# Optimization experiments

Hardware: AMD Instinct MI355X
Metric: run time of the kernel (lower is better)

The kernel has to match this reference:

```python
import jax, jax.numpy as jnp
import numpy as np

BOUND = 1.0
N_RAYS = 2048
TOT = 128        # num_steps (samples per pixel)
IND_S = 16       # indicator_steps
MAX_DEPTHS = 2
HID = 64
EPS = 1e-8


def setup_inputs() -> dict:
    key = jax.random.key(0)
    ks = jax.random.split(key, 13)
    M = N_RAYS * TOT
    rays_o = 0.3 * jax.random.normal(ks[0], (N_RAYS, 3), jnp.float32)
    rd = jax.random.normal(ks[1], (N_RAYS, 3), jnp.float32)
    rays_d = rd / (jnp.linalg.norm(rd, axis=-1, keepdims=True) + EPS)
    env_map = 0.1 * jax.random.normal(ks[2], (3, 128, 256), jnp.float32)
    Wd1 = jax.random.normal(ks[3], (3, HID), jnp.float32) / np.sqrt(3.0)
    Wd2 = jax.random.normal(ks[4], (HID, 3), jnp.float32) / np.sqrt(HID)
    Wf1 = jax.random.normal(ks[5], (6, HID), jnp.float32) / np.sqrt(6.0)
    Ws = jax.random.normal(ks[6], (HID, 3), jnp.float32) / np.sqrt(HID)
    Wdir = jax.random.normal(ks[7], (HID, 3), jnp.float32) / np.sqrt(HID)
    Wrho = jax.random.normal(ks[8], (HID, 3), jnp.float32) / np.sqrt(HID)
    jitter = jax.random.uniform(ks[9], (MAX_DEPTHS, M, IND_S), jnp.float32)
    u_t = jax.random.uniform(ks[10], (MAX_DEPTHS, M), jnp.float32)
    u_scatter = jax.random.uniform(ks[11], (MAX_DEPTHS, M), jnp.float32)
    channel = jax.random.randint(ks[12], (MAX_DEPTHS, M), 0, 3)
    return dict(rays_o=rays_o, rays_d=rays_d, env_map=env_map, Wd1=Wd1, Wd2=Wd2,
                Wf1=Wf1, Ws=Ws, Wdir=Wdir, Wrho=Wrho,
                jitter=jitter, u_t=u_t, u_scatter=u_scatter, channel=channel)


def _density(pts, Wd1, Wd2):
    # stand-in NeRF density field: 3 spectral channels, positive
    return jax.nn.softplus(jnp.sin(pts @ Wd1) @ Wd2)


def _material(o, d, Wf1, Ws, Wdir, Wrho):
    f = jnp.tanh(jnp.concatenate([o, d], axis=-1) @ Wf1)
    sigma_t = jax.nn.softplus(f @ Ws)                     # [M,3]
    dn = f @ Wdir
    d_out = dn / (jnp.linalg.norm(dn, axis=-1, keepdims=True) + EPS)
    fused_rho = jax.nn.sigmoid(f @ Wrho)                  # [M,3]
    return sigma_t, d_out, fused_rho


def _sample_env(env_map, p):
    # equirectangular lookup == torch grid_sample(bilinear, align_corners=False, zero pad)
    x, y, z = p[:, 0], p[:, 1], p[:, 2]
    theta = jnp.nan_to_num(jnp.arctan2(x, -z)) / jnp.pi            # grid x in [-1,1]
    phi = 2.0 / jnp.pi * jnp.nan_to_num(jnp.arccos(y)) - 1.0       # grid y in [-1,1]
    C, H, W = env_map.shape
    ix = ((theta + 1.0) * W - 1.0) * 0.5
    iy = ((phi + 1.0) * H - 1.0) * 0.5
    x0 = jnp.floor(ix); y0 = jnp.floor(iy)
    wx = ix - x0; wy = iy - y0

    def tap(xc, yc, w):
        inb = (xc >= 0) & (xc < W) & (yc >= 0) & (yc < H)
        xi = jnp.clip(xc, 0, W - 1).astype(jnp.int32)
        yi = jnp.clip(yc, 0, H - 1).astype(jnp.int32)
        return (w * inb)[:, None] * env_map[:, yi, xi].T   # [M,3]

    v = (tap(x0, y0, (1 - wx) * (1 - wy)) + tap(x0 + 1, y0, wx * (1 - wy)) +
         tap(x0, y0 + 1, (1 - wx) * wy) + tap(x0 + 1, y0 + 1, wx * wy))
    return jnp.exp(v)


def _render(rays_o, rays_d, env_map, Wd1, Wd2, Wf1, Ws, Wdir, Wrho,
            jitter, u_t, u_scatter, channel):
    M = N_RAYS * TOT
    o = jnp.repeat(rays_o, TOT, axis=0)   # [M,3]
    d = jnp.repeat(rays_d, TOT, axis=0)
    alive = jnp.ones((M,), bool)          # masked version of boolean compaction
    thr = jnp.ones((M, 3), jnp.float32)
    rgbs = jnp.zeros((M, 3), jnp.float32)
    lin = jnp.linspace(0.0, 1.0, IND_S)

    for dep in range(MAX_DEPTHS):
        # ray-sphere intersection (radius=bound)
        a = jnp.sum(d * d, -1)
        b = 2.0 * jnp.sum(d * o, -1)
        c = jnp.sum(o * o, -1) - BOUND ** 2
        delta = b * b - 4.0 * a * c
        alive = alive & (delta > 0.0)
        sq = jnp.sqrt(jnp.maximum(delta, 0.0))
        nears = jnp.maximum((-b - sq) / (2.0 * a), 0.001)
        fars = jnp.maximum((-b + sq) / (2.0 * a), 0.001)
        span = fars - nears

        # stratified indicator samples -> per-channel majorant
        z = nears[:, None] + span[:, None] * lin[None, :]
        z = z + (jitter[dep] - 0.5) * (span[:, None] / IND_S)
        pts = o[:, None, :] + d[:, None, :] * z[:, :, None]          # [M,S,3]
        sigma = _density(pts.reshape(-1, 3), Wd1, Wd2).reshape(M, IND_S, 3)
        ch = channel[dep]
        maj_multi = jnp.maximum(sigma.max(axis=1), 0.001)            # [M,3]
        sig_ch = jnp.take_along_axis(sigma, ch[:, None, None], axis=2)[..., 0]
        maj = jnp.maximum(sig_ch.max(axis=1), 0.001)                 # [M]

        # free-flight sampling (last depth forces hit at far boundary)
        if dep < MAX_DEPTHS - 1:
            t = -jnp.log1p(-u_t[dep]) / maj + nears
        else:
            t = fars
        hit = alive & (t >= fars)

        # environment hit contribution
        denom = jnp.exp(-maj_multi * span[:, None]) / (maj_multi.max(-1, keepdims=True) + EPS) + EPS
        Le = _sample_env(env_map, o + d * fars[:, None])
        contrib = thr * (denom / jax.lax.stop_gradient(denom.mean(-1, keepdims=True))) * Le
        rgbs = rgbs + jnp.where(hit[:, None], contrib, 0.0)
        alive = alive & ~hit
        if dep == MAX_DEPTHS - 1:
            break

        # throughput update + null/real scattering (delta tracking)
        trans = jnp.exp(-maj_multi * (t - nears)[:, None]) / maj_multi.max(-1, keepdims=True)
        den2 = jax.lax.stop_gradient((maj_multi * trans).mean(-1, keepdims=True))
        thr = jnp.where(alive[:, None], thr * trans / den2, thr)
        o = jnp.where(alive[:, None], jax.lax.stop_gradient(o + d * t[:, None]), o)
        sigma_t, d_out, fused_rho = _material(o, d, Wf1, Ws, Wdir, Wrho)
        sp = jnp.minimum(jnp.take_along_axis(sigma_t, ch[:, None], axis=1)[:, 0] / maj, 1.0)
        sm = alive & (u_scatter[dep] < sp)
        d = jnp.where(sm[:, None], d_out, d)
        thr = jnp.where(sm[:, None], thr / (sp[:, None] + EPS) * fused_rho,
              jnp.where(alive[:, None], thr / (1.0 - sp[:, None] + EPS), thr))

    return rgbs.reshape(N_RAYS, TOT, 3).mean(axis=1)   # [N,3]


def reference(rays_o, rays_d, env_map, Wd1, Wd2, Wf1, Ws, Wdir, Wrho,
              jitter, u_t, u_scatter, channel):
    return _render(rays_o, rays_d, env_map, Wd1, Wd2, Wf1, Ws, Wdir, Wrho,
                   jitter, u_t, u_scatter, channel)
```

## Files before the change

### kernel.cpp

```cpp
#include <hip/hip_runtime.h>
#include <math.h>

#define NRAYS 2048
#define TOT   128
#define INDS  16
#define HID   64
#define EPSF  1e-8f
#define MTOT  (NRAYS*TOT)
#define NTAB  128

typedef float f32x2 __attribute__((ext_vector_type(2)));
typedef float f32x4 __attribute__((ext_vector_type(4)));

__device__ __forceinline__ float rcp_f(float x) {
    return __builtin_amdgcn_rcpf(x);
}
__device__ __forceinline__ float softplus_f(float x) {
    return fmaxf(x, 0.0f) + __logf(1.0f + __expf(-fabsf(x)));
}
__device__ __forceinline__ float sigmoid_f(float x) {
    return rcp_f(1.0f + __expf(-x));
}
__device__ __forceinline__ float tanh_fast(float x) {
    float e2 = __expf(2.0f * x);
    return 1.0f - 2.0f * rcp_f(e2 + 1.0f);
}
__device__ __forceinline__ f32x2 pkmax(f32x2 a, f32x2 b) {
    f32x2 r; r.x = fmaxf(a.x, b.x); r.y = fmaxf(a.y, b.y); return r;
}
__device__ __forceinline__ f32x2 pkfma(f32x2 a, f32x2 b, f32x2 c) {
    return __builtin_elementwise_fma(a, b, c);
}

__device__ __forceinline__ float atan_poly(float r) {
    float r2 = r*r;
    float p = -0.0117212f;
    p = fmaf(p, r2,  0.05265332f);
    p = fmaf(p, r2, -0.11643287f);
    p = fmaf(p, r2,  0.19354346f);
    p = fmaf(p, r2, -0.33262347f);
    p = fmaf(p, r2,  0.99997726f);
    return r * p;
}
__device__ __forceinline__ float atan2_fast(float y, float x) {
    float ay = fabsf(y), ax = fabsf(x);
    float mx = fmaxf(ay, ax), mn = fminf(ay, ax);
    float r  = mn * rcp_f(fmaxf(mx, 1e-30f));
    float t  = atan_poly(r);
    t = (ay > ax) ? (1.57079632679f - t) : t;
    t = (x < 0.0f) ? (3.14159265359f - t) : t;
    return (y < 0.0f) ? -t : t;
}
__device__ __forceinline__ float acos_fast(float x) {
    float ax = fabsf(x);
    float p = -0.0187293f;
    p = fmaf(p, ax,  0.0742610f);
    p = fmaf(p, ax, -0.2121144f);
    p = fmaf(p, ax,  1.5707288f);
    float s = sqrtf(1.0f - ax) * p;
    return (x < 0.0f) ? (3.14159265359f - s) : s;
}

#define CK(i) ((float)(i)*(1.0f/15.0f) - 0.03125f)

#define MAKE_Z(jA, jB, kbase, nears, span)                                    \
    float s16 = (span) * (1.0f/16.0f);                                        \
    f32x2 z01, z23, z45, z67;                                                 \
    z01.x = fmaf((jA).x, s16, fmaf(span, CK((kbase)+0), nears));              \
    z01.y = fmaf((jA).y, s16, fmaf(span, CK((kbase)+1), nears));              \
    z23.x = fmaf((jA).z, s16, fmaf(span, CK((kbase)+2), nears));              \
    z23.y = fmaf((jA).w, s16, fmaf(span, CK((kbase)+3), nears));              \
    z45.x = fmaf((jB).x, s16, fmaf(span, CK((kbase)+4), nears));              \
    z45.y = fmaf((jB).y, s16, fmaf(span, CK((kbase)+5), nears));              \
    z67.x = fmaf((jB).z, s16, fmaf(span, CK((kbase)+6), nears));              \
    z67.y = fmaf((jB).w, s16, fmaf(span, CK((kbase)+7), nears));

#define TAB_EVAL(zz, mx0, mx1, mx2)                                           \
    {                                                                         \
        float x = ((zz) - ztab0) * invh;                                      \
        x = fminf(fmaxf(x, 0.0f), (float)(NTAB-1) - 1e-3f);                   \
        int i = (int)x; float w = x - (float)i;                               \
        float ta0 = sT0[i], tb0 = sT0[i+1];                                   \
        float ta1 = sT1[i], tb1 = sT1[i+1];                                   \
        float ta2 = sT2[i], tb2 = sT2[i+1];                                   \
        mx0 = fmaxf(mx0, fmaf(w, tb0 - ta0, ta0));                            \
        mx1 = fmaxf(mx1, fmaf(w, tb1 - ta1, ta1));                            \
        mx2 = fmaxf(mx2, fmaf(w, tb2 - ta2, ta2));                            \
    }

__device__ __forceinline__ void env_logv(
    const float* __restrict__ env_map,
    float px, float py, float pz,
    float& v0, float& v1, float& v2)
{
    float theta = atan2_fast(px, -pz) * (1.0f/3.14159265358979323846f);
    float acv = (fabsf(py) <= 1.0f) ? acos_fast(py) : 0.0f;
    float phi = 0.63661977236758134308f * acv - 1.0f;
    float ixf = ((theta + 1.0f)*256.0f - 1.0f)*0.5f;
    float iyf = ((phi   + 1.0f)*128.0f - 1.0f)*0.5f;
    float x0f = floorf(ixf), y0f = floorf(iyf);
    float wx = ixf - x0f, wy = iyf - y0f;
    v0 = 0.f; v1 = 0.f; v2 = 0.f;
    auto tap = [&](float xc, float yc, float w) {
        if (xc >= 0.0f && xc < 256.0f && yc >= 0.0f && yc < 128.0f) {
            int xi = (int)xc, yi = (int)yc;
            const float* e = env_map + yi*256 + xi;
            v0 += w * e[0];
            v1 += w * e[128*256];
            v2 += w * e[2*128*256];
        }
    };
    tap(x0f,      y0f,      (1.0f-wx)*(1.0f-wy));
    tap(x0f+1.0f, y0f,      wx*(1.0f-wy));
    tap(x0f,      y0f+1.0f, (1.0f-wx)*wy);
    tap(x0f+1.0f, y0f+1.0f, wx*wy);
}

__global__ __launch_bounds__(256)
void render_kernel(const float* __restrict__ rays_o,
                   const float* __restrict__ rays_d,
                   const float* __restrict__ env_map,
                   const float* __restrict__ Wd1,
                   const float* __restrict__ Wd2,
                   const float* __restrict__ Wf1,
                   const float* __restrict__ Ws,
                   const float* __restrict__ Wdir,
                   const float* __restrict__ Wrho,
                   const float* __restrict__ jitter,
                   const float* __restrict__ u_t,
                   const float* __restrict__ u_scatter,
                   const int*   __restrict__ channel,
                   float* __restrict__ out)
{
    const int ray  = blockIdx.x;
    const int tid  = threadIdx.x;
    const int s    = tid >> 1;
    const int half = tid & 1;
    const int m    = ray * TOT + s;
    const int kbase = half * 8;

    __shared__ f32x4 sAB[HID];
    __shared__ f32x4 sW01[HID];
    __shared__ f32x2 sW2[HID];
    __shared__ f32x4 sPW[HID];
    __shared__ f32x4 sM0[HID];
    __shared__ f32x4 sM1[HID];
    __shared__ f32x4 sM2[HID];
    __shared__ float sT0[NTAB];
    __shared__ float sT1[NTAB];
    __shared__ float sT2[NTAB];
    __shared__ f32x4 sP0[TOT];
    __shared__ f32x4 sP1[TOT];
    __shared__ f32x2 sP2[TOT];
    __shared__ float sEnvE[3];
    __shared__ int   sCnt;
    __shared__ float sred[4][3];

    const float4* j0p = (const float4*)(jitter + (size_t)m*INDS + kbase);
    float4 j0A = j0p[0], j0B = j0p[1];
    const float4* j1p = (const float4*)(jitter + ((size_t)MTOT + m)*INDS + kbase);
    float4 j1A = j1p[0], j1B = j1p[1];
    int   ch = channel[m];
    float ut = u_t[m];
    float us = u_scatter[m];

    float ox = rays_o[ray*3+0], oy = rays_o[ray*3+1], oz = rays_o[ray*3+2];
    float dx = rays_d[ray*3+0], dy = rays_d[ray*3+1], dz = rays_d[ray*3+2];

    if (tid == 0) sCnt = 0;
    if (tid < HID) {
        const float INV2PI = 0.15915494309189535f;
        float w1x = Wd1[tid], w1y = Wd1[HID+tid], w1z = Wd1[2*HID+tid];
        float pw1x = w1x*INV2PI, pw1y = w1y*INV2PI, pw1z = w1z*INV2PI;
        float A = ox*pw1x + oy*pw1y + oz*pw1z;
        float B = dx*pw1x + dy*pw1y + dz*pw1z;
        float w20 = Wd2[3*tid], w21 = Wd2[3*tid+1], w22 = Wd2[3*tid+2];
        sAB[tid]  = (f32x4){A, A, B, B};
        sW01[tid] = (f32x4){w20, w20, w21, w21};
        sW2[tid]  = (f32x2){w22, w22};
        sPW[tid]  = (f32x4){pw1x, pw1y, pw1z, 0.0f};
        float f0 = Wf1[tid],       f1 = Wf1[HID+tid],   f2 = Wf1[2*HID+tid];
        float f3 = Wf1[3*HID+tid], f4 = Wf1[4*HID+tid], f5 = Wf1[5*HID+tid];
        float P = ox*f0 + oy*f1 + oz*f2 + dx*f3 + dy*f4 + dz*f5;
        float Q = dx*f0 + dy*f1 + dz*f2;
        sM0[tid] = (f32x4){P, Q, Ws[3*tid], Ws[3*tid+1]};
        sM1[tid] = (f32x4){Ws[3*tid+2], Wdir[3*tid], Wdir[3*tid+1], Wdir[3*tid+2]};
        sM2[tid] = (f32x4){Wrho[3*tid], Wrho[3*tid+1], Wrho[3*tid+2], 0.0f};
    }
    __syncthreads();

    float a0g = dx*dx + dy*dy + dz*dz;
    float b0g = 2.0f*(dx*ox + dy*oy + dz*oz);
    float c0g = (ox*ox + oy*oy + oz*oz) - 1.0f;
    float delta0 = b0g*b0g - 4.0f*a0g*c0g;
    bool alive = (delta0 > 0.0f);

    float nears = 0.f, fars = 0.f, span = 0.f, ztab0 = 0.f, invh = 0.f;
    if (alive) {
        float sq = sqrtf(delta0);
        float inv2a = rcp_f(a0g + a0g);
        nears = fmaxf((-b0g - sq) * inv2a, 0.001f);
        fars  = fmaxf((-b0g + sq) * inv2a, 0.001f);
        span  = fars - nears;
        ztab0 = fmaf(-span, 0.03125f, nears);
        float width = span * 1.0625f;
        float hstep = width * (1.0f/(NTAB-1));
        invh = (float)(NTAB-1) * rcp_f(width);
        int p = tid >> 1;
        float zp = fmaf((float)p, hstep, ztab0);
        float f0 = 0.f, f1 = 0.f, f2 = 0.f;
        const int jb = half * 32;
        #pragma unroll 4
        for (int j = jb; j < jb + 32; ++j) {
            f32x4 ab  = sAB[j];
            f32x4 w01 = sW01[j];
            f32x2 w2  = sW2[j];
            float hv = __builtin_amdgcn_sinf(fmaf(zp, ab.z, ab.x));
            f0 = fmaf(hv, w01.x, f0);
            f1 = fmaf(hv, w01.z, f1);
            f2 = fmaf(hv, w2.x, f2);
        }
        f0 += __shfl_xor(f0, 1, 64);
        f1 += __shfl_xor(f1, 1, 64);
        f2 += __shfl_xor(f2, 1, 64);
        if (half == 0) { sT0[p] = f0; sT1[p] = f1; sT2[p] = f2; }
        if (tid == 0) {
            float v0,v1,v2;
            env_logv(env_map, fmaf(dx,fars,ox), fmaf(dy,fars,oy), fmaf(dz,fars,oz),
                     v0,v1,v2);
            sEnvE[0] = __expf(v0); sEnvE[1] = __expf(v1); sEnvE[2] = __expf(v2);
        }
    }
    __syncthreads();

    float thr0 = 1.f, thr1 = 1.f, thr2 = 1.f;
    float rgb0 = 0.f, rgb1 = 0.f, rgb2 = 0.f;
    bool  tab_d1 = false;
    float tadv = 0.f;

    if (alive) {
        MAKE_Z(j0A, j0B, kbase, nears, span)
        float mx0 = -1e30f, mx1 = -1e30f, mx2 = -1e30f;
        TAB_EVAL(z01.x, mx0,mx1,mx2) TAB_EVAL(z01.y, mx0,mx1,mx2)
        TAB_EVAL(z23.x, mx0,mx1,mx2) TAB_EVAL(z23.y, mx0,mx1,mx2)
        TAB_EVAL(z45.x, mx0,mx1,mx2) TAB_EVAL(z45.y, mx0,mx1,mx2)
        TAB_EVAL(z67.x, mx0,mx1,mx2) TAB_EVAL(z67.y, mx0,mx1,mx2)
        mx0 = fmaxf(mx0, __shfl_xor(mx0, 1, 64));
        mx1 = fmaxf(mx1, __shfl_xor(mx1, 1, 64));
        mx2 = fmaxf(mx2, __shfl_xor(mx2, 1, 64));

        float maj0 = fmaxf(softplus_f(mx0), 0.001f);
        float maj1 = fmaxf(softplus_f(mx1), 0.001f);
        float maj2 = fmaxf(softplus_f(mx2), 0.001f);
        float mmax = fmaxf(fmaxf(maj0, maj1), maj2);

        float maj = (ch == 0) ? maj0 : ((ch == 1) ? maj1 : maj2);
        float t   = fmaf(-__logf(1.0f - ut), rcp_f(maj), nears);

        if (t >= fars) {
            float im   = rcp_f(mmax + EPSF);
            float den0 = fmaf(__expf(-maj0*span), im, EPSF);
            float den1 = fmaf(__expf(-maj1*span), im, EPSF);
            float den2 = fmaf(__expf(-maj2*span), im, EPSF);
            float idm = 3.0f * rcp_f(den0+den1+den2);
            rgb0 = den0*idm*sEnvE[0];
            rgb1 = den1*idm*sEnvE[1];
            rgb2 = den2*idm*sEnvE[2];
        } else {
            float tn  = t - nears;
            float imm = rcp_f(mmax);
            float tr0 = __expf(-maj0*tn) * imm;
            float tr1 = __expf(-maj1*tn) * imm;
            float tr2 = __expf(-maj2*tn) * imm;
            float i2m = 3.0f * rcp_f(maj0*tr0 + maj1*tr1 + maj2*tr2);
            thr0 = tr0 * i2m;
            thr1 = tr1 * i2m;
            thr2 = tr2 * i2m;
            ox = fmaf(dx, t, ox); oy = fmaf(dy, t, oy); oz = fmaf(dz, t, oz);

            float st0=0.f, st1=0.f, st2=0.f;
            float dn0=0.f, dn1=0.f, dn2v=0.f;
            float rh0=0.f, rh1=0.f, rh2=0.f;
            const int j0 = half * 32;
            #pragma unroll 2
            for (int j = j0; j < j0 + 32; ++j) {
                f32x4 q0 = sM0[j];
                f32x4 q1 = sM1[j];
                f32x4 q2 = sM2[j];
                float pre = fmaf(t, q0.y, q0.x);
                float f = tanh_fast(pre);
                st0  = fmaf(f, q0.z, st0);
                st1  = fmaf(f, q0.w, st1);
                st2  = fmaf(f, q1.x, st2);
                dn0  = fmaf(f, q1.y, dn0);
                dn1  = fmaf(f, q1.z, dn1);
                dn2v = fmaf(f, q1.w, dn2v);
                rh0  = fmaf(f, q2.x, rh0);
                rh1  = fmaf(f, q2.y, rh1);
                rh2  = fmaf(f, q2.z, rh2);
            }
            st0  += __shfl_xor(st0, 1, 64);
            st1  += __shfl_xor(st1, 1, 64);
            st2  += __shfl_xor(st2, 1, 64);
            dn0  += __shfl_xor(dn0, 1, 64);
            dn1  += __shfl_xor(dn1, 1, 64);
            dn2v += __shfl_xor(dn2v, 1, 64);
            rh0  += __shfl_xor(rh0, 1, 64);
            rh1  += __shfl_xor(rh1, 1, 64);
            rh2  += __shfl_xor(rh2, 1, 64);

            float stch = (ch == 0) ? st0 : ((ch == 1) ? st1 : st2);
            float sp = fminf(softplus_f(stch) * rcp_f(maj), 1.0f);
            if (us < sp) {
                float inr = rcp_f(sqrtf(dn0*dn0 + dn1*dn1 + dn2v*dn2v) + EPSF);
                float ndx = dn0*inr, ndy = dn1*inr, ndz = dn2v*inr;
                float isp = rcp_f(sp + EPSF);
                float t0 = thr0 * isp * sigmoid_f(rh0);
                float t1 = thr1 * isp * sigmoid_f(rh1);
                float t2 = thr2 * isp * sigmoid_f(rh2);
                if (half == 0) {
                    int sl = atomicAdd(&sCnt, 1);
                    sP0[sl] = (f32x4){ox, oy, oz, ndx};
                    sP1[sl] = (f32x4){ndy, ndz, t0, t1};
                    sP2[sl] = (f32x2){t2, (float)m};
                }
            } else {
                float iv = rcp_f(1.0f - sp + EPSF);
                thr0 *= iv; thr1 *= iv; thr2 *= iv;
                tab_d1 = true;
                tadv = t;
            }
        }
    }
    __syncthreads();
    int npool = sCnt;

    if (tab_d1) {
        float fars1 = fmaxf(fars - tadv, 0.001f);
        float span1 = fars1 - 0.001f;
        float n1    = tadv + 0.001f;
        MAKE_Z(j1A, j1B, kbase, n1, span1)
        float mx0 = -1e30f, mx1 = -1e30f, mx2 = -1e30f;
        TAB_EVAL(z01.x, mx0,mx1,mx2) TAB_EVAL(z01.y, mx0,mx1,mx2)
        TAB_EVAL(z23.x, mx0,mx1,mx2) TAB_EVAL(z23.y, mx0,mx1,mx2)
        TAB_EVAL(z45.x, mx0,mx1,mx2) TAB_EVAL(z45.y, mx0,mx1,mx2)
        TAB_EVAL(z67.x, mx0,mx1,mx2) TAB_EVAL(z67.y, mx0,mx1,mx2)
        mx0 = fmaxf(mx0, __shfl_xor(mx0, 1, 64));
        mx1 = fmaxf(mx1, __shfl_xor(mx1, 1, 64));
        mx2 = fmaxf(mx2, __shfl_xor(mx2, 1, 64));

        float maj0 = fmaxf(softplus_f(mx0), 0.001f);
        float maj1 = fmaxf(softplus_f(mx1), 0.001f);
        float maj2 = fmaxf(softplus_f(mx2), 0.001f);
        float mmax = fmaxf(fmaxf(maj0, maj1), maj2);

        float im   = rcp_f(mmax + EPSF);
        float den0 = fmaf(__expf(-maj0*span1), im, EPSF);
        float den1 = fmaf(__expf(-maj1*span1), im, EPSF);
        float den2 = fmaf(__expf(-maj2*span1), im, EPSF);
        float idm = 3.0f * rcp_f(den0+den1+den2);
        rgb0 += thr0 * den0*idm*sEnvE[0];
        rgb1 += thr1 * den1*idm*sEnvE[1];
        rgb2 += thr2 * den2*idm*sEnvE[2];
    }

    {
        const int qlane = tid & 3;
        const int kq    = qlane * 4;
        const float kqf = (float)kq;
        for (int q = tid >> 2; q < npool; q += 64) {
            f32x4 p0 = sP0[q];
            f32x4 p1 = sP1[q];
            f32x2 p2 = sP2[q];
            float pox = p0.x, poy = p0.y, poz = p0.z;
            float pdx = p0.w, pdy = p1.x, pdz = p1.y;
            float pt0 = p1.z, pt1 = p1.w, pt2 = p2.x;
            int   mm  = (int)p2.y;

            const float4* jp = (const float4*)(jitter + ((size_t)MTOT + mm)*INDS + kq);
            float4 jq = jp[0];

            float a1 = pdx*pdx + pdy*pdy + pdz*pdz;
            float b1 = 2.0f*(pdx*pox + pdy*poy + pdz*poz);
            float c1 = (pox*pox + poy*poy + poz*poz) - 1.0f;
            float delta1 = b1*b1 - 4.0f*a1*c1;
            if (delta1 > 0.0f) {
                float sq1    = sqrtf(delta1);
                float inv2a1 = rcp_f(a1 + a1);
                float nears1 = fmaxf((-b1 - sq1) * inv2a1, 0.001f);
                float fars1  = fmaxf((-b1 + sq1) * inv2a1, 0.001f);
                float span1  = fars1 - nears1;
                float s16q   = span1 * (1.0f/16.0f);
                f32x2 zA, zB;
                zA.x = fmaf(jq.x, s16q, fmaf(span1, (kqf+0.0f)*(1.0f/15.0f) - 0.03125f, nears1));
                zA.y = fmaf(jq.y, s16q, fmaf(span1, (kqf+1.0f)*(1.0f/15.0f) - 0.03125f, nears1));
                zB.x = fmaf(jq.z, s16q, fmaf(span1, (kqf+2.0f)*(1.0f/15.0f) - 0.03125f, nears1));
                zB.y = fmaf(jq.w, s16q, fmaf(span1, (kqf+3.0f)*(1.0f/15.0f) - 0.03125f, nears1));

                f32x2 a0A = {0.f,0.f}, a0B = {0.f,0.f};
                f32x2 a1A = {0.f,0.f}, a1B = {0.f,0.f};
                f32x2 a2A = {0.f,0.f}, a2B = {0.f,0.f};
                #pragma unroll 4
                for (int j = 0; j < HID; ++j) {
                    f32x4 pw  = sPW[j];
                    f32x4 w01 = sW01[j];
                    f32x2 w2  = sW2[j];
                    float A = fmaf(pox, pw.x, fmaf(poy, pw.y, poz*pw.z));
                    float B = fmaf(pdx, pw.x, fmaf(pdy, pw.y, pdz*pw.z));
                    f32x2 A2 = {A, A}, B2 = {B, B};
                    f32x2 gA = pkfma(zA, B2, A2);
                    f32x2 gB = pkfma(zB, B2, A2);
                    f32x2 hA, hB;
                    hA.x = __builtin_amdgcn_sinf(gA.x); hA.y = __builtin_amdgcn_sinf(gA.y);
                    hB.x = __builtin_amdgcn_sinf(gB.x); hB.y = __builtin_amdgcn_sinf(gB.y);
                    f32x2 W0 = {w01.x, w01.y}, W1 = {w01.z, w01.w};
                    a0A = pkfma(hA, W0, a0A); a0B = pkfma(hB, W0, a0B);
                    a1A = pkfma(hA, W1, a1A); a1B = pkfma(hB, W1, a1B);
                    a2A = pkfma(hA, w2, a2A); a2B = pkfma(hB, w2, a2B);
                }
                f32x2 pm0 = pkmax(a0A, a0B);
                f32x2 pm1 = pkmax(a1A, a1B);
                f32x2 pm2 = pkmax(a2A, a2B);
                float mx0 = fmaxf(pm0.x, pm0.y);
                float mx1 = fmaxf(pm1.x, pm1.y);
                float mx2 = fmaxf(pm2.x, pm2.y);
                mx0 = fmaxf(mx0, __shfl_xor(mx0, 1, 64));
                mx1 = fmaxf(mx1, __shfl_xor(mx1, 1, 64));
                mx2 = fmaxf(mx2, __shfl_xor(mx2, 1, 64));
                mx0 = fmaxf(mx0, __shfl_xor(mx0, 2, 64));
                mx1 = fmaxf(mx1, __shfl_xor(mx1, 2, 64));
                mx2 = fmaxf(mx2, __shfl_xor(mx2, 2, 64));

                float maj0 = fmaxf(softplus_f(mx0), 0.001f);
                float maj1 = fmaxf(softplus_f(mx1), 0.001f);
                float maj2 = fmaxf(softplus_f(mx2), 0.001f);
                float mmax = fmaxf(fmaxf(maj0, maj1), maj2);

                float im   = rcp_f(mmax + EPSF);
                float den0 = fmaf(__expf(-maj0*span1), im, EPSF);
                float den1 = fmaf(__expf(-maj1*span1), im, EPSF);
                float den2 = fmaf(__expf(-maj2*span1), im, EPSF);
                float idm = 3.0f * rcp_f(den0+den1+den2);
                float v0,v1,v2;
                env_logv(env_map, fmaf(pdx,fars1,pox), fmaf(pdy,fars1,poy),
                         fmaf(pdz,fars1,poz), v0,v1,v2);
                if (qlane < 2) {
                    rgb0 += pt0 * den0*idm*__expf(v0);
                    rgb1 += pt1 * den1*idm*__expf(v1);
                    rgb2 += pt2 * den2*idm*__expf(v2);
                }
            }
        }
    }

    float r0 = rgb0, r1 = rgb1, r2 = rgb2;
    #pragma unroll
    for (int off = 32; off > 0; off >>= 1) {
        r0 += __shfl_down(r0, off, 64);
        r1 += __shfl_down(r1, off, 64);
        r2 += __shfl_down(r2, off, 64);
    }
    int wave = tid >> 6;
    if ((tid & 63) == 0) {
        sred[wave][0] = r0; sred[wave][1] = r1; sred[wave][2] = r2;
    }
    __syncthreads();
    if (tid == 0) {
        out[ray*3+0] = (sred[0][0]+sred[1][0]+sred[2][0]+sred[3][0]) * (1.0f/256.0f);
        out[ray*3+1] = (sred[0][1]+sred[1][1]+sred[2][1]+sred[3][1]) * (1.0f/256.0f);
        out[ray*3+2] = (sred[0][2]+sred[1][2]+sred[2][2]+sred[3][2]) * (1.0f/256.0f);
    }
}

extern "C" void kernel_launch(void* const* d_in, const int* in_sizes, int n_in,
                              void* d_out, int out_size, void* d_ws, size_t ws_size,
                              hipStream_t stream) {
    const float* rays_o    = (const float*)d_in[0];
    const float* rays_d    = (const float*)d_in[1];
    const float* env_map   = (const float*)d_in[2];
    const float* Wd1       = (const float*)d_in[3];
    const float* Wd2       = (const float*)d_in[4];
    const float* Wf1       = (const float*)d_in[5];
    const float* Ws        = (const float*)d_in[6];
    const float* Wdir      = (const float*)d_in[7];
    const float* Wrho      = (const float*)d_in[8];
    const float* jitter    = (const float*)d_in[9];
    const float* u_t       = (const float*)d_in[10];
    const float* u_scatter = (const float*)d_in[11];
    const int*   channel   = (const int*)d_in[12];
    float* out = (float*)d_out;

    render_kernel<<<dim3(NRAYS), dim3(256), 0, stream>>>(
        rays_o, rays_d, env_map, Wd1, Wd2, Wf1, Ws, Wdir, Wrho,
        jitter, u_t, u_scatter, channel, out);
}
```

Measured before the change: 160.6 us.

## Evaluate scattered-ray second bounce inline instead of compacted shared-memory pool

```diff
diff --git a/kernel.cpp b/kernel.cpp
--- a/kernel.cpp
+++ b/kernel.cpp
@@ -149,11 +149,7 @@
     __shared__ float sT0[NTAB];
     __shared__ float sT1[NTAB];
     __shared__ float sT2[NTAB];
-    __shared__ f32x4 sP0[TOT];
-    __shared__ f32x4 sP1[TOT];
-    __shared__ f32x2 sP2[TOT];
     __shared__ float sEnvE[3];
-    __shared__ int   sCnt;
     __shared__ float sred[4][3];
 
     const float4* j0p = (const float4*)(jitter + (size_t)m*INDS + kbase);
@@ -167,7 +163,6 @@
     float ox = rays_o[ray*3+0], oy = rays_o[ray*3+1], oz = rays_o[ray*3+2];
     float dx = rays_d[ray*3+0], dy = rays_d[ray*3+1], dz = rays_d[ray*3+2];
 
-    if (tid == 0) sCnt = 0;
     if (tid < HID) {
         const float INV2PI = 0.15915494309189535f;
         float w1x = Wd1[tid], w1y = Wd1[HID+tid], w1z = Wd1[2*HID+tid];
@@ -315,14 +310,77 @@
                 float inr = rcp_f(sqrtf(dn0*dn0 + dn1*dn1 + dn2v*dn2v) + EPSF);
                 float ndx = dn0*inr, ndy = dn1*inr, ndz = dn2v*inr;
                 float isp = rcp_f(sp + EPSF);
-                float t0 = thr0 * isp * sigmoid_f(rh0);
-                float t1 = thr1 * isp * sigmoid_f(rh1);
-                float t2 = thr2 * isp * sigmoid_f(rh2);
-                if (half == 0) {
-                    int sl = atomicAdd(&sCnt, 1);
-                    sP0[sl] = (f32x4){ox, oy, oz, ndx};
-                    sP1[sl] = (f32x4){ndy, ndz, t0, t1};
-                    sP2[sl] = (f32x2){t2, (float)m};
+                thr0 = thr0 * isp * sigmoid_f(rh0);
+                thr1 = thr1 * isp * sigmoid_f(rh1);
+                thr2 = thr2 * isp * sigmoid_f(rh2);
+
+                float a1 = ndx*ndx + ndy*ndy + ndz*ndz;
+                float b1 = 2.0f*(ndx*ox + ndy*oy + ndz*oz);
+                float c1v = (ox*ox + oy*oy + oz*oz) - 1.0f;
+                float delta1 = b1*b1 - 4.0f*a1*c1v;
+                if (delta1 > 0.0f) {
+                    float sq1    = sqrtf(delta1);
+                    float inv2a1 = rcp_f(a1 + a1);
+                    float nears1 = fmaxf((-b1 - sq1) * inv2a1, 0.001f);
+                    float fars1  = fmaxf((-b1 + sq1) * inv2a1, 0.001f);
+                    float span1  = fars1 - nears1;
+                    MAKE_Z(j1A, j1B, kbase, nears1, span1)
+
+                    f32x2 c0a={0.f,0.f}, c0b={0.f,0.f}, c0c={0.f,0.f}, c0d={0.f,0.f};
+                    f32x2 c1a={0.f,0.f}, c1b={0.f,0.f}, c1c={0.f,0.f}, c1d={0.f,0.f};
+                    f32x2 c2a={0.f,0.f}, c2b={0.f,0.f}, c2c={0.f,0.f}, c2d={0.f,0.f};
+                    #pragma unroll 4
+                    for (int j = 0; j < HID; ++j) {
+                        f32x4 pw  = sPW[j];
+                        f32x4 w01 = sW01[j];
+                        f32x2 w2  = sW2[j];
+                        float A = fmaf(ox, pw.x, fmaf(oy, pw.y, oz*pw.z));
+                        float B = fmaf(ndx, pw.x, fmaf(ndy, pw.y, ndz*pw.z));
+                        f32x2 A2 = {A, A}, B2 = {B, B};
+                        f32x2 g01 = pkfma(z01, B2, A2);
+                        f32x2 g23 = pkfma(z23, B2, A2);
+                        f32x2 g45 = pkfma(z45, B2, A2);
+                        f32x2 g67 = pkfma(z67, B2, A2);
+                        f32x2 h01, h23, h45, h67;
+                        h01.x = __builtin_amdgcn_sinf(g01.x); h01.y = __builtin_amdgcn_sinf(g01.y);
+                        h23.x = __builtin_amdgcn_sinf(g23.x); h23.y = __builtin_amdgcn_sinf(g23.y);
+                        h45.x = __builtin_amdgcn_sinf(g45.x); h45.y = __builtin_amdgcn_sinf(g45.y);
+                        h67.x = __builtin_amdgcn_sinf(g67.x); h67.y = __builtin_amdgcn_sinf(g67.y);
+                        f32x2 W0 = {w01.x, w01.y};
+                        f32x2 W1 = {w01.z, w01.w};
+                        c0a = pkfma(h01, W0, c0a); c0b = pkfma(h23, W0, c0b);
+                        c0c = pkfma(h45, W0, c0c); c0d = pkfma(h67, W0, c0d);
+                        c1a = pkfma(h01, W1, c1a); c1b = pkfma(h23, W1, c1b);
+                        c1c = pkfma(h45, W1, c1c); c1d = pkfma(h67, W1, c1d);
+                        c2a = pkfma(h01, w2, c2a); c2b = pkfma(h23, w2, c2b);
+                        c2c = pkfma(h45, w2, c2c); c2d = pkfma(h67, w2, c2d);
+                    }
+                    f32x2 pm0 = pkmax(pkmax(c0a, c0b), pkmax(c0c, c0d));
+                    f32x2 pm1 = pkmax(pkmax(c1a, c1b), pkmax(c1c, c1d));
+                    f32x2 pm2 = pkmax(pkmax(c2a, c2b), pkmax(c2c, c2d));
+                    float my0 = fmaxf(pm0.x, pm0.y);
+                    float my1 = fmaxf(pm1.x, pm1.y);
+                    float my2 = fmaxf(pm2.x, pm2.y);
+                    my0 = fmaxf(my0, __shfl_xor(my0, 1, 64));
+                    my1 = fmaxf(my1, __shfl_xor(my1, 1, 64));
+                    my2 = fmaxf(my2, __shfl_xor(my2, 1, 64));
+
+                    float mj0 = fmaxf(softplus_f(my0), 0.001f);
+                    float mj1 = fmaxf(softplus_f(my1), 0.001f);
+                    float mj2 = fmaxf(softplus_f(my2), 0.001f);
+                    float mmax1 = fmaxf(fmaxf(mj0, mj1), mj2);
+
+                    float im1  = rcp_f(mmax1 + EPSF);
+                    float dn0e = fmaf(__expf(-mj0*span1), im1, EPSF);
+                    float dn1e = fmaf(__expf(-mj1*span1), im1, EPSF);
+                    float dn2e = fmaf(__expf(-mj2*span1), im1, EPSF);
+                    float idm1 = 3.0f * rcp_f(dn0e+dn1e+dn2e);
+                    float v0,v1,v2;
+                    env_logv(env_map, fmaf(ndx,fars1,ox), fmaf(ndy,fars1,oy),
+                             fmaf(ndz,fars1,oz), v0,v1,v2);
+                    rgb0 += thr0 * dn0e*idm1*__expf(v0);
+                    rgb1 += thr1 * dn1e*idm1*__expf(v1);
+                    rgb2 += thr2 * dn2e*idm1*__expf(v2);
                 }
             } else {
                 float iv = rcp_f(1.0f - sp + EPSF);
@@ -332,8 +390,6 @@
             }
         }
     }
-    __syncthreads();
-    int npool = sCnt;
 
     if (tab_d1) {
         float fars1 = fmaxf(fars - tadv, 0.001f);
@@ -362,95 +418,6 @@
         rgb0 += thr0 * den0*idm*sEnvE[0];
         rgb1 += thr1 * den1*idm*sEnvE[1];
         rgb2 += thr2 * den2*idm*sEnvE[2];
-    }
-
-    {
-        const int qlane = tid & 3;
-        const int kq    = qlane * 4;
-        const float kqf = (float)kq;
-        for (int q = tid >> 2; q < npool; q += 64) {
-            f32x4 p0 = sP0[q];
-            f32x4 p1 = sP1[q];
-            f32x2 p2 = sP2[q];
-            float pox = p0.x, poy = p0.y, poz = p0.z;
-            float pdx = p0.w, pdy = p1.x, pdz = p1.y;
-            float pt0 = p1.z, pt1 = p1.w, pt2 = p2.x;
-            int   mm  = (int)p2.y;
-
-            const float4* jp = (const float4*)(jitter + ((size_t)MTOT + mm)*INDS + kq);
-            float4 jq = jp[0];
-
-            float a1 = pdx*pdx + pdy*pdy + pdz*pdz;
-            float b1 = 2.0f*(pdx*pox + pdy*poy + pdz*poz);
-            float c1 = (pox*pox + poy*poy + poz*poz) - 1.0f;
-            float delta1 = b1*b1 - 4.0f*a1*c1;
-            if (delta1 > 0.0f) {
-                float sq1    = sqrtf(delta1);
-                float inv2a1 = rcp_f(a1 + a1);
-                float nears1 = fmaxf((-b1 - sq1) * inv2a1, 0.001f);
-                float fars1  = fmaxf((-b1 + sq1) * inv2a1, 0.001f);
-                float span1  = fars1 - nears1;
-                float s16q   = span1 * (1.0f/16.0f);
-                f32x2 zA, zB;
-                zA.x = fmaf(jq.x, s16q, fmaf(span1, (kqf+0.0f)*(1.0f/15.0f) - 0.03125f, nears1));
-                zA.y = fmaf(jq.y, s16q, fmaf(span1, (kqf+1.0f)*(1.0f/15.0f) - 0.03125f, nears1));
-                zB.x = fmaf(jq.z, s16q, fmaf(span1, (kqf+2.0f)*(1.0f/15.0f) - 0.03125f, nears1));
-                zB.y = fmaf(jq.w, s16q, fmaf(span1, (kqf+3.0f)*(1.0f/15.0f) - 0.03125f, nears1));
-
-                f32x2 a0A = {0.f,0.f}, a0B = {0.f,0.f};
-                f32x2 a1A = {0.f,0.f}, a1B = {0.f,0.f};
-                f32x2 a2A = {0.f,0.f}, a2B = {0.f,0.f};
-                #pragma unroll 4
-                for (int j = 0; j < HID; ++j) {
-                    f32x4 pw  = sPW[j];
-                    f32x4 w01 = sW01[j];
-                    f32x2 w2  = sW2[j];
-                    float A = fmaf(pox, pw.x, fmaf(poy, pw.y, poz*pw.z));
-                    float B = fmaf(pdx, pw.x, fmaf(pdy, pw.y, pdz*pw.z));
-                    f32x2 A2 = {A, A}, B2 = {B, B};
-                    f32x2 gA = pkfma(zA, B2, A2);
-                    f32x2 gB = pkfma(zB, B2, A2);
-                    f32x2 hA, hB;
-                    hA.x = __builtin_amdgcn_sinf(gA.x); hA.y = __builtin_amdgcn_sinf(gA.y);
-                    hB.x = __builtin_amdgcn_sinf(gB.x); hB.y = __builtin_amdgcn_sinf(gB.y);
-                    f32x2 W0 = {w01.x, w01.y}, W1 = {w01.z, w01.w};
-                    a0A = pkfma(hA, W0, a0A); a0B = pkfma(hB, W0, a0B);
-                    a1A = pkfma(hA, W1, a1A); a1B = pkfma(hB, W1, a1B);
-                    a2A = pkfma(hA, w2, a2A); a2B = pkfma(hB, w2, a2B);
-                }
-                f32x2 pm0 = pkmax(a0A, a0B);
-                f32x2 pm1 = pkmax(a1A, a1B);
-                f32x2 pm2 = pkmax(a2A, a2B);
-                float mx0 = fmaxf(pm0.x, pm0.y);
-                float mx1 = fmaxf(pm1.x, pm1.y);
-                float mx2 = fmaxf(pm2.x, pm2.y);
-                mx0 = fmaxf(mx0, __shfl_xor(mx0, 1, 64));
-                mx1 = fmaxf(mx1, __shfl_xor(mx1, 1, 64));
-                mx2 = fmaxf(mx2, __shfl_xor(mx2, 1, 64));
-                mx0 = fmaxf(mx0, __shfl_xor(mx0, 2, 64));
-                mx1 = fmaxf(mx1, __shfl_xor(mx1, 2, 64));
-                mx2 = fmaxf(mx2, __shfl_xor(mx2, 2, 64));
-
-                float maj0 = fmaxf(softplus_f(mx0), 0.001f);
-                float maj1 = fmaxf(softplus_f(mx1), 0.001f);
-                float maj2 = fmaxf(softplus_f(mx2), 0.001f);
-                float mmax = fmaxf(fmaxf(maj0, maj1), maj2);
-
-                float im   = rcp_f(mmax + EPSF);
-                float den0 = fmaf(__expf(-maj0*span1), im, EPSF);
-                float den1 = fmaf(__expf(-maj1*span1), im, EPSF);
-                float den2 = fmaf(__expf(-maj2*span1), im, EPSF);
-                float idm = 3.0f * rcp_f(den0+den1+den2);
-                float v0,v1,v2;
-                env_logv(env_map, fmaf(pdx,fars1,pox), fmaf(pdy,fars1,poy),
-                         fmaf(pdz,fars1,poz), v0,v1,v2);
-                if (qlane < 2) {
-                    rgb0 += pt0 * den0*idm*__expf(v0);
-                    rgb1 += pt1 * den1*idm*__expf(v1);
-                    rgb2 += pt2 * den2*idm*__expf(v2);
-                }
-            }
-        }
     }
 
     float r0 = rgb0, r1 = rgb1, r2 = rgb2;
```

New measurement: 163.6 us. About the same (+1.8%).

## Read MLP weights directly from global memory instead of staging in LDS

Applied to the files above, without the earlier changes.

```diff
diff --git a/kernel.cpp b/kernel.cpp
--- a/kernel.cpp
+++ b/kernel.cpp
@@ -75,17 +75,15 @@
     z67.x = fmaf((jB).z, s16, fmaf(span, CK((kbase)+6), nears));              \
     z67.y = fmaf((jB).w, s16, fmaf(span, CK((kbase)+7), nears));
 
-#define TAB_EVAL(zz, mx0, mx1, mx2)                                           \
+#define TAB_EVAL4(zz, mx0, mx1, mx2)                                          \
     {                                                                         \
         float x = ((zz) - ztab0) * invh;                                      \
         x = fminf(fmaxf(x, 0.0f), (float)(NTAB-1) - 1e-3f);                   \
         int i = (int)x; float w = x - (float)i;                               \
-        float ta0 = sT0[i], tb0 = sT0[i+1];                                   \
-        float ta1 = sT1[i], tb1 = sT1[i+1];                                   \
-        float ta2 = sT2[i], tb2 = sT2[i+1];                                   \
-        mx0 = fmaxf(mx0, fmaf(w, tb0 - ta0, ta0));                            \
-        mx1 = fmaxf(mx1, fmaf(w, tb1 - ta1, ta1));                            \
-        mx2 = fmaxf(mx2, fmaf(w, tb2 - ta2, ta2));                            \
+        f32x4 ta = sT4[i], tb = sT4[i+1];                                     \
+        mx0 = fmaxf(mx0, fmaf(w, tb.x - ta.x, ta.x));                         \
+        mx1 = fmaxf(mx1, fmaf(w, tb.y - ta.y, ta.y));                         \
+        mx2 = fmaxf(mx2, fmaf(w, tb.z - ta.z, ta.z));                         \
     }
 
 __device__ __forceinline__ void env_logv(
@@ -139,16 +137,7 @@
     const int m    = ray * TOT + s;
     const int kbase = half * 8;
 
-    __shared__ f32x4 sAB[HID];
-    __shared__ f32x4 sW01[HID];
-    __shared__ f32x2 sW2[HID];
-    __shared__ f32x4 sPW[HID];
-    __shared__ f32x4 sM0[HID];
-    __shared__ f32x4 sM1[HID];
-    __shared__ f32x4 sM2[HID];
-    __shared__ float sT0[NTAB];
-    __shared__ float sT1[NTAB];
-    __shared__ float sT2[NTAB];
+    __shared__ f32x4 sT4[NTAB];
     __shared__ f32x4 sP0[TOT];
     __shared__ f32x4 sP1[TOT];
     __shared__ f32x2 sP2[TOT];
@@ -167,27 +156,11 @@
     float ox = rays_o[ray*3+0], oy = rays_o[ray*3+1], oz = rays_o[ray*3+2];
     float dx = rays_d[ray*3+0], dy = rays_d[ray*3+1], dz = rays_d[ray*3+2];
 
+    const float INV2PI = 0.15915494309189535f;
+    float oxs = ox*INV2PI, oys = oy*INV2PI, ozs = oz*INV2PI;
+    float dxs = dx*INV2PI, dys = dy*INV2PI, dzs = dz*INV2PI;
+
     if (tid == 0) sCnt = 0;
-    if (tid < HID) {
-        const float INV2PI = 0.15915494309189535f;
-        float w1x = Wd1[tid], w1y = Wd1[HID+tid], w1z = Wd1[2*HID+tid];
-        float pw1x = w1x*INV2PI, pw1y = w1y*INV2PI, pw1z = w1z*INV2PI;
-        float A = ox*pw1x + oy*pw1y + oz*pw1z;
-        float B = dx*pw1x + dy*pw1y + dz*pw1z;
-        float w20 = Wd2[3*tid], w21 = Wd2[3*tid+1], w22 = Wd2[3*tid+2];
-        sAB[tid]  = (f32x4){A, A, B, B};
-        sW01[tid] = (f32x4){w20, w20, w21, w21};
-        sW2[tid]  = (f32x2){w22, w22};
-        sPW[tid]  = (f32x4){pw1x, pw1y, pw1z, 0.0f};
-        float f0 = Wf1[tid],       f1 = Wf1[HID+tid],   f2 = Wf1[2*HID+tid];
-        float f3 = Wf1[3*HID+tid], f4 = Wf1[4*HID+tid], f5 = Wf1[5*HID+tid];
-        float P = ox*f0 + oy*f1 + oz*f2 + dx*f3 + dy*f4 + dz*f5;
-        float Q = dx*f0 + dy*f1 + dz*f2;
-        sM0[tid] = (f32x4){P, Q, Ws[3*tid], Ws[3*tid+1]};
-        sM1[tid] = (f32x4){Ws[3*tid+2], Wdir[3*tid], Wdir[3*tid+1], Wdir[3*tid+2]};
-        sM2[tid] = (f32x4){Wrho[3*tid], Wrho[3*tid+1], Wrho[3*tid+2], 0.0f};
-    }
-    __syncthreads();
 
     float a0g = dx*dx + dy*dy + dz*dz;
     float b0g = 2.0f*(dx*ox + dy*oy + dz*oz);
@@ -212,18 +185,18 @@
         const int jb = half * 32;
         #pragma unroll 4
         for (int j = jb; j < jb + 32; ++j) {
-            f32x4 ab  = sAB[j];
-            f32x4 w01 = sW01[j];
-            f32x2 w2  = sW2[j];
-            float hv = __builtin_amdgcn_sinf(fmaf(zp, ab.z, ab.x));
-            f0 = fmaf(hv, w01.x, f0);
-            f1 = fmaf(hv, w01.z, f1);
-            f2 = fmaf(hv, w2.x, f2);
+            float w1x = Wd1[j], w1y = Wd1[HID+j], w1z = Wd1[2*HID+j];
+            float dotO = fmaf(oxs, w1x, fmaf(oys, w1y, ozs*w1z));
+            float dotD = fmaf(dxs, w1x, fmaf(dys, w1y, dzs*w1z));
+            float hv = __builtin_amdgcn_sinf(fmaf(zp, dotD, dotO));
+            f0 = fmaf(hv, Wd2[3*j+0], f0);
+            f1 = fmaf(hv, Wd2[3*j+1], f1);
+            f2 = fmaf(hv, Wd2[3*j+2], f2);
         }
         f0 += __shfl_xor(f0, 1, 64);
         f1 += __shfl_xor(f1, 1, 64);
         f2 += __shfl_xor(f2, 1, 64);
-        if (half == 0) { sT0[p] = f0; sT1[p] = f1; sT2[p] = f2; }
+        if (half == 0) sT4[p] = (f32x4){f0, f1, f2, 0.0f};
         if (tid == 0) {
             float v0,v1,v2;
             env_logv(env_map, fmaf(dx,fars,ox), fmaf(dy,fars,oy), fmaf(dz,fars,oz),
@@ -241,10 +214,10 @@
     if (alive) {
         MAKE_Z(j0A, j0B, kbase, nears, span)
         float mx0 = -1e30f, mx1 = -1e30f, mx2 = -1e30f;
-        TAB_EVAL(z01.x, mx0,mx1,mx2) TAB_EVAL(z01.y, mx0,mx1,mx2)
-        TAB_EVAL(z23.x, mx0,mx1,mx2) TAB_EVAL(z23.y, mx0,mx1,mx2)
-        TAB_EVAL(z45.x, mx0,mx1,mx2) TAB_EVAL(z45.y, mx0,mx1,mx2)
-        TAB_EVAL(z67.x, mx0,mx1,mx2) TAB_EVAL(z67.y, mx0,mx1,mx2)
+        TAB_EVAL4(z01.x, mx0,mx1,mx2) TAB_EVAL4(z01.y, mx0,mx1,mx2)
+        TAB_EVAL4(z23.x, mx0,mx1,mx2) TAB_EVAL4(z23.y, mx0,mx1,mx2)
+        TAB_EVAL4(z45.x, mx0,mx1,mx2) TAB_EVAL4(z45.y, mx0,mx1,mx2)
+        TAB_EVAL4(z67.x, mx0,mx1,mx2) TAB_EVAL4(z67.y, mx0,mx1,mx2)
         mx0 = fmaxf(mx0, __shfl_xor(mx0, 1, 64));
         mx1 = fmaxf(mx1, __shfl_xor(mx1, 1, 64));
         mx2 = fmaxf(mx2, __shfl_xor(mx2, 1, 64));
@@ -276,7 +249,9 @@
             thr0 = tr0 * i2m;
             thr1 = tr1 * i2m;
             thr2 = tr2 * i2m;
-            ox = fmaf(dx, t, ox); oy = fmaf(dy, t, oy); oz = fmaf(dz, t, oz);
+            float oxn = fmaf(dx, t, ox);
+            float oyn = fmaf(dy, t, oy);
+            float ozn = fmaf(dz, t, oz);
 
             float st0=0.f, st1=0.f, st2=0.f;
             float dn0=0.f, dn1=0.f, dn2v=0.f;
@@ -284,20 +259,21 @@
             const int j0 = half * 32;
             #pragma unroll 2
             for (int j = j0; j < j0 + 32; ++j) {
-                f32x4 q0 = sM0[j];
-                f32x4 q1 = sM1[j];
-                f32x4 q2 = sM2[j];
-                float pre = fmaf(t, q0.y, q0.x);
-                float f = tanh_fast(pre);
-                st0  = fmaf(f, q0.z, st0);
-                st1  = fmaf(f, q0.w, st1);
-                st2  = fmaf(f, q1.x, st2);
-                dn0  = fmaf(f, q1.y, dn0);
-                dn1  = fmaf(f, q1.z, dn1);
-                dn2v = fmaf(f, q1.w, dn2v);
-                rh0  = fmaf(f, q2.x, rh0);
-                rh1  = fmaf(f, q2.y, rh1);
-                rh2  = fmaf(f, q2.z, rh2);
+                float fA = Wf1[j],         fB = Wf1[HID+j],   fC = Wf1[2*HID+j];
+                float fD = Wf1[3*HID+j],   fE = Wf1[4*HID+j], fF = Wf1[5*HID+j];
+                float P = fmaf(ox,fA, fmaf(oy,fB, fmaf(oz,fC,
+                          fmaf(dx,fD, fmaf(dy,fE, dz*fF)))));
+                float Q = fmaf(dx,fA, fmaf(dy,fB, dz*fC));
+                float f = tanh_fast(fmaf(t, Q, P));
+                st0  = fmaf(f, Ws[3*j+0],   st0);
+                st1  = fmaf(f, Ws[3*j+1],   st1);
+                st2  = fmaf(f, Ws[3*j+2],   st2);
+                dn0  = fmaf(f, Wdir[3*j+0], dn0);
+                dn1  = fmaf(f, Wdir[3*j+1], dn1);
+                dn2v = fmaf(f, Wdir[3*j+2], dn2v);
+                rh0  = fmaf(f, Wrho[3*j+0], rh0);
+                rh1  = fmaf(f, Wrho[3*j+1], rh1);
+                rh2  = fmaf(f, Wrho[3*j+2], rh2);
             }
             st0  += __shfl_xor(st0, 1, 64);
             st1  += __shfl_xor(st1, 1, 64);
@@ -320,7 +296,7 @@
                 float t2 = thr2 * isp * sigmoid_f(rh2);
                 if (half == 0) {
                     int sl = atomicAdd(&sCnt, 1);
-                    sP0[sl] = (f32x4){ox, oy, oz, ndx};
+                    sP0[sl] = (f32x4){oxn, oyn, ozn, ndx};
                     sP1[sl] = (f32x4){ndy, ndz, t0, t1};
                     sP2[sl] = (f32x2){t2, (float)m};
                 }
@@ -341,10 +317,10 @@
         float n1    = tadv + 0.001f;
         MAKE_Z(j1A, j1B, kbase, n1, span1)
         float mx0 = -1e30f, mx1 = -1e30f, mx2 = -1e30f;
-        TAB_EVAL(z01.x, mx0,mx1,mx2) TAB_EVAL(z01.y, mx0,mx1,mx2)
-        TAB_EVAL(z23.x, mx0,mx1,mx2) TAB_EVAL(z23.y, mx0,mx1,mx2)
-        TAB_EVAL(z45.x, mx0,mx1,mx2) TAB_EVAL(z45.y, mx0,mx1,mx2)
-        TAB_EVAL(z67.x, mx0,mx1,mx2) TAB_EVAL(z67.y, mx0,mx1,mx2)
+        TAB_EVAL4(z01.x, mx0,mx1,mx2) TAB_EVAL4(z01.y, mx0,mx1,mx2)
+        TAB_EVAL4(z23.x, mx0,mx1,mx2) TAB_EVAL4(z23.y, mx0,mx1,mx2)
+        TAB_EVAL4(z45.x, mx0,mx1,mx2) TAB_EVAL4(z45.y, mx0,mx1,mx2)
+        TAB_EVAL4(z67.x, mx0,mx1,mx2) TAB_EVAL4(z67.y, mx0,mx1,mx2)
         mx0 = fmaxf(mx0, __shfl_xor(mx0, 1, 64));
         mx1 = fmaxf(mx1, __shfl_xor(mx1, 1, 64));
         mx2 = fmaxf(mx2, __shfl_xor(mx2, 1, 64));
@@ -397,26 +373,28 @@
                 zB.x = fmaf(jq.z, s16q, fmaf(span1, (kqf+2.0f)*(1.0f/15.0f) - 0.03125f, nears1));
                 zB.y = fmaf(jq.w, s16q, fmaf(span1, (kqf+3.0f)*(1.0f/15.0f) - 0.03125f, nears1));
 
+                float poxs = pox*INV2PI, poys = poy*INV2PI, pozs = poz*INV2PI;
+                float pdxs = pdx*INV2PI, pdys = pdy*INV2PI, pdzs = pdz*INV2PI;
+
                 f32x2 a0A = {0.f,0.f}, a0B = {0.f,0.f};
                 f32x2 a1A = {0.f,0.f}, a1B = {0.f,0.f};
                 f32x2 a2A = {0.f,0.f}, a2B = {0.f,0.f};
                 #pragma unroll 4
                 for (int j = 0; j < HID; ++j) {
-                    f32x4 pw  = sPW[j];
-                    f32x4 w01 = sW01[j];
-                    f32x2 w2  = sW2[j];
-                    float A = fmaf(pox, pw.x, fmaf(poy, pw.y, poz*pw.z));
-                    float B = fmaf(pdx, pw.x, fmaf(pdy, pw.y, pdz*pw.z));
+                    float w1x = Wd1[j], w1y = Wd1[HID+j], w1z = Wd1[2*HID+j];
+                    float w20 = Wd2[3*j+0], w21 = Wd2[3*j+1], w22 = Wd2[3*j+2];
+                    float A = fmaf(poxs, w1x, fmaf(poys, w1y, pozs*w1z));
+                    float B = fmaf(pdxs, w1x, fmaf(pdys, w1y, pdzs*w1z));
                     f32x2 A2 = {A, A}, B2 = {B, B};
                     f32x2 gA = pkfma(zA, B2, A2);
                     f32x2 gB = pkfma(zB, B2, A2);
                     f32x2 hA, hB;
                     hA.x = __builtin_amdgcn_sinf(gA.x); hA.y = __builtin_amdgcn_sinf(gA.y);
                     hB.x = __builtin_amdgcn_sinf(gB.x); hB.y = __builtin_amdgcn_sinf(gB.y);
-                    f32x2 W0 = {w01.x, w01.y}, W1 = {w01.z, w01.w};
+                    f32x2 W0 = {w20, w20}, W1 = {w21, w21}, W2v = {w22, w22};
                     a0A = pkfma(hA, W0, a0A); a0B = pkfma(hB, W0, a0B);
                     a1A = pkfma(hA, W1, a1A); a1B = pkfma(hB, W1, a1B);
-                    a2A = pkfma(hA, w2, a2A); a2B = pkfma(hB, w2, a2B);
+                    a2A = pkfma(hA, W2v, a2A); a2B = pkfma(hB, W2v, a2B);
                 }
                 f32x2 pm0 = pkmax(a0A, a0B);
                 f32x2 pm1 = pkmax(a1A, a1B);
```

Result: slower. 214.7 us (+33.7%).
